# Kernel optimization log

Hardware: AMD Instinct MI355X
Metric: run time of the kernel (lower is better)

## Reference

```python
import jax, jax.numpy as jnp
import numpy as np

K0 = 16
TAU = -2.053748910631823
EPS = 1e-06


def setup_inputs() -> dict:
    key = jax.random.key(0)
    k1, k2, k3 = jax.random.split(key, 3)
    B, DIN, DOUT = 32768, 1024, 1024
    x = jax.random.normal(k1, (B, DIN), dtype=jnp.float32)
    weight = jax.random.normal(k2, (DOUT, DIN), dtype=jnp.float32) * 0.02
    bias = jax.random.normal(k3, (DOUT,), dtype=jnp.float32) * 0.02
    return {"x": x, "weight": weight, "bias": bias}


def reference(x, weight, bias):
    # Kernel loads x and w as fp16 and accumulates in fp32.
    x16 = x.astype(jnp.float16)        # [B, DIN]
    w16 = weight.astype(jnp.float16)   # [DOUT, DIN]

    xa, wa = x16[:, :K0], w16[:, :K0]
    # Warmup partial dot product over the first K0 columns: y1[b,n] = sum_k x[b,k]*w[n,k]
    y1 = jnp.einsum("bk,nk->bn", xa, wa, preferred_element_type=jnp.float32)
    # s2[b,n] = sum_k (x[b,k]*w[n,k])^2 = sum_k x^2 * w^2
    s2 = jnp.einsum("bk,nk->bn", xa * xa, wa * wa, preferred_element_type=jnp.float32)

    denom = jnp.sqrt(s2 / (K0 + EPS) + EPS)
    tstat = jnp.abs(y1) / jnp.maximum(denom, EPS)
    passed = tstat < TAU                     # early-terminate mask (true => skip remaining cols)
    still_active = ~passed                   # [B, DOUT]

    # Remaining columns contribute only where still_active.
    rest = jnp.einsum("bk,nk->bn", x16[:, K0:], w16[:, K0:], preferred_element_type=jnp.float32)
    acc = y1 + rest * still_active.astype(jnp.float32)

    out = acc + bias.astype(jnp.float32)
    return out.astype(x.dtype)
```

## Files before the change

kernel.cpp:

```cpp
#include <hip/hip_runtime.h>

typedef _Float16 f16;
typedef f16 f16x2 __attribute__((ext_vector_type(2)));
typedef f16 f16x4 __attribute__((ext_vector_type(4)));
typedef f16 f16x8 __attribute__((ext_vector_type(8)));
typedef float f32x4 __attribute__((ext_vector_type(4)));

constexpr int Mdim = 32768, Ndim = 1024, Kdim = 1024;
constexpr int BM = 256, BN = 256, BK = 64;
constexpr int NT = Kdim / BK;

static __device__ inline f16x2 cvt2(float a, float b) {
    return __builtin_bit_cast(f16x2, __builtin_amdgcn_cvt_pkrtz(a, b));
}
static __device__ inline f16x4 cvt4(float4 v) {
    f16x2 lo = cvt2(v.x, v.y), hi = cvt2(v.z, v.w);
    return __builtin_shufflevector(lo, hi, 0, 1, 2, 3);
}

__global__ __launch_bounds__(512, 2)
void etrow_gemm(const float* __restrict__ X, const float* __restrict__ W,
                const float* __restrict__ bias, float* __restrict__ out)
{
    __shared__ f16 As[2][BM * BK];
    __shared__ f16 Bs[2][BN * BK];

    const int bid = blockIdx.x;
    const int cpx = gridDim.x >> 3;
    const int wg  = (bid & 7) * cpx + (bid >> 3);
    const int mIdx = wg >> 2;
    const int nIdx = wg & 3;

    const int tid  = threadIdx.x;
    const int lane = tid & 63;
    const int wave = tid >> 6;
    const int wr   = (wave >> 2) * 128;
    const int wc   = (wave & 3) * 64;

    const int r0 = tid >> 4;
    const int c4 = tid & 15;

    const float* Xb = X + (size_t)mIdx * BM * Kdim;
    const float* Wb = W + (size_t)nIdx * BN * Kdim;

    float4 S[8];
    f32x4 acc[8][4] = {};

    auto loadA = [&](int kt) {
        const float* xa = Xb + kt * BK + c4 * 4;
        #pragma unroll
        for (int p = 0; p < 8; ++p)
            S[p] = *(const float4*)(xa + (p * 32 + r0) * Kdim);
    };
    auto loadB = [&](int kt) {
        const float* wb = Wb + kt * BK + c4 * 4;
        #pragma unroll
        for (int p = 0; p < 8; ++p)
            S[p] = *(const float4*)(wb + (p * 32 + r0) * Kdim);
    };
    auto cvtWrite = [&](f16* lds) {
        #pragma unroll
        for (int p = 0; p < 8; ++p) {
            const int r = p * 32 + r0;
            const int byte = (r * (BK * 2) + c4 * 8) ^ ((r & 7) << 4);
            *(f16x4*)((char*)lds + byte) = cvt4(S[p]);
        }
    };

    auto computeSub = [&](const f16* Ab, const f16* Bb, int s) {
        f16x8 af[8], bf[4];
        const int kb = s * 64 + (lane >> 4) * 16;
        #pragma unroll
        for (int i = 0; i < 8; ++i) {
            const int r = wr + i * 16 + (lane & 15);
            const int byte = (r * (BK * 2) + kb) ^ ((r & 7) << 4);
            af[i] = *(const f16x8*)((const char*)Ab + byte);
        }
        #pragma unroll
        for (int j = 0; j < 4; ++j) {
            const int r = wc + j * 16 + (lane & 15);
            const int byte = (r * (BK * 2) + kb) ^ ((r & 7) << 4);
            bf[j] = *(const f16x8*)((const char*)Bb + byte);
        }
        #pragma unroll
        for (int i = 0; i < 8; ++i)
            #pragma unroll
            for (int j = 0; j < 4; ++j)
                acc[i][j] = __builtin_amdgcn_mfma_f32_16x16x32_f16(
                    af[i], bf[j], acc[i][j], 0, 0, 0);
    };

    loadA(0); cvtWrite(&As[0][0]);
    loadB(0); cvtWrite(&Bs[0][0]);
    loadA(1);
    __syncthreads();

    for (int t = 0; t < NT; ++t) {
        const int cur = t & 1, nxt = cur ^ 1;
        if (t + 1 < NT) { cvtWrite(&As[nxt][0]); loadB(t + 1); }
        computeSub(&As[cur][0], &Bs[cur][0], 0);
        if (t + 1 < NT) { cvtWrite(&Bs[nxt][0]); }
        if (t + 2 < NT) { loadA(t + 2); }
        computeSub(&As[cur][0], &Bs[cur][0], 1);
        __syncthreads();
    }

    const int col0  = nIdx * BN + wc + (lane & 15);
    const int rbase = mIdx * BM + wr + (lane >> 4) * 4;
    float bv[4];
    #pragma unroll
    for (int n = 0; n < 4; ++n) bv[n] = bias[col0 + n * 16];

    #pragma unroll
    for (int m = 0; m < 8; ++m) {
        #pragma unroll
        for (int j = 0; j < 4; ++j) {
            const int row = rbase + m * 16 + j;
            float* o = out + (size_t)row * Ndim + col0;
            #pragma unroll
            for (int n = 0; n < 4; ++n)
                o[n * 16] = acc[m][n][j] + bv[n];
        }
    }
}

extern "C" void kernel_launch(void* const* d_in, const int* in_sizes, int n_in,
                              void* d_out, int out_size, void* d_ws, size_t ws_size,
                              hipStream_t stream) {
    const float* X  = (const float*)d_in[0];
    const float* W  = (const float*)d_in[1];
    const float* bs = (const float*)d_in[2];
    float* out = (float*)d_out;
    const int grid = (Mdim / BM) * (Ndim / BN);
    etrow_gemm<<<grid, 512, 0, stream>>>(X, W, bs, out);
}
```

Measured before the change: 96.74 us.

## Restructure K-loop into four barrier-synchronized phases with MFMA priority boosting

Splits each K-tile's compute into four phases of two 16-row sub-tiles, with workgroup barriers and s_setprio raised around the MFMA bursts. The A and B global loads, conversions and LDS writes for the next tile are interleaved between those phases. A and B staging now use separate register arrays (SA/SB), so both next-tile loads can be in flight at once. The aim is to hide global-load and LDS-write latency behind matrix work and keep waves in lockstep. In exchange it adds more barriers per tile and more registers, which risks spills or lower occupancy.

After: 150.6 us. +55.6%, slower.

```diff
diff --git a/kernel.cpp b/kernel.cpp
--- a/kernel.cpp
+++ b/kernel.cpp
@@ -16,6 +16,11 @@
 static __device__ inline f16x4 cvt4(float4 v) {
     f16x2 lo = cvt2(v.x, v.y), hi = cvt2(v.z, v.w);
     return __builtin_shufflevector(lo, hi, 0, 1, 2, 3);
+}
+static __device__ inline void bar() {
+    asm volatile("" ::: "memory");
+    __builtin_amdgcn_s_barrier();
+    asm volatile("" ::: "memory");
 }
 
 __global__ __launch_bounds__(512, 2)
@@ -43,66 +48,90 @@
     const float* Xb = X + (size_t)mIdx * BM * Kdim;
     const float* Wb = W + (size_t)nIdx * BN * Kdim;
 
-    float4 S[8];
+    float4 SA[8], SB[8];
     f32x4 acc[8][4] = {};
 
-    auto loadA = [&](int kt) {
-        const float* xa = Xb + kt * BK + c4 * 4;
+    auto issueA = [&](int kt) {
+        const float* p = Xb + kt * BK + c4 * 4;
         #pragma unroll
-        for (int p = 0; p < 8; ++p)
-            S[p] = *(const float4*)(xa + (p * 32 + r0) * Kdim);
+        for (int q = 0; q < 8; ++q)
+            SA[q] = *(const float4*)(p + (q * 32 + r0) * Kdim);
     };
-    auto loadB = [&](int kt) {
-        const float* wb = Wb + kt * BK + c4 * 4;
+    auto issueB = [&](int kt) {
+        const float* p = Wb + kt * BK + c4 * 4;
         #pragma unroll
-        for (int p = 0; p < 8; ++p)
-            S[p] = *(const float4*)(wb + (p * 32 + r0) * Kdim);
+        for (int q = 0; q < 8; ++q)
+            SB[q] = *(const float4*)(p + (q * 32 + r0) * Kdim);
     };
-    auto cvtWrite = [&](f16* lds) {
+    auto cvtWrA = [&](f16* lds) {
         #pragma unroll
-        for (int p = 0; p < 8; ++p) {
-            const int r = p * 32 + r0;
-            const int byte = (r * (BK * 2) + c4 * 8) ^ ((r & 7) << 4);
-            *(f16x4*)((char*)lds + byte) = cvt4(S[p]);
+        for (int q = 0; q < 8; ++q) {
+            const int r = q * 32 + r0;
+            const int byte = (r * 128 + c4 * 8) ^ ((r & 7) << 4);
+            *(f16x4*)((char*)lds + byte) = cvt4(SA[q]);
+        }
+    };
+    auto cvtWrB = [&](f16* lds) {
+        #pragma unroll
+        for (int q = 0; q < 8; ++q) {
+            const int r = q * 32 + r0;
+            const int byte = (r * 128 + c4 * 8) ^ ((r & 7) << 4);
+            *(f16x4*)((char*)lds + byte) = cvt4(SB[q]);
         }
     };
 
-    auto computeSub = [&](const f16* Ab, const f16* Bb, int s) {
-        f16x8 af[8], bf[4];
-        const int kb = s * 64 + (lane >> 4) * 16;
+    auto phase = [&](const f16* Ac, const f16* Bc, int m0) {
+        f16x8 af[2][2];
         #pragma unroll
-        for (int i = 0; i < 8; ++i) {
-            const int r = wr + i * 16 + (lane & 15);
-            const int byte = (r * (BK * 2) + kb) ^ ((r & 7) << 4);
-            af[i] = *(const f16x8*)((const char*)Ab + byte);
+        for (int mi = 0; mi < 2; ++mi)
+            #pragma unroll
+            for (int s = 0; s < 2; ++s) {
+                const int r = wr + (m0 + mi) * 16 + (lane & 15);
+                const int byte = (r * 128 + s * 64 + (lane >> 4) * 16) ^ ((r & 7) << 4);
+                af[mi][s] = *(const f16x8*)((const char*)Ac + byte);
+            }
+        bar();
+        __builtin_amdgcn_s_setprio(1);
+        #pragma unroll
+        for (int s = 0; s < 2; ++s) {
+            f16x8 bf[4];
+            #pragma unroll
+            for (int j = 0; j < 4; ++j) {
+                const int r = wc + j * 16 + (lane & 15);
+                const int byte = (r * 128 + s * 64 + (lane >> 4) * 16) ^ ((r & 7) << 4);
+                bf[j] = *(const f16x8*)((const char*)Bc + byte);
+            }
+            #pragma unroll
+            for (int mi = 0; mi < 2; ++mi)
+                #pragma unroll
+                for (int j = 0; j < 4; ++j)
+                    acc[m0 + mi][j] = __builtin_amdgcn_mfma_f32_16x16x32_f16(
+                        af[mi][s], bf[j], acc[m0 + mi][j], 0, 0, 0);
         }
-        #pragma unroll
-        for (int j = 0; j < 4; ++j) {
-            const int r = wc + j * 16 + (lane & 15);
-            const int byte = (r * (BK * 2) + kb) ^ ((r & 7) << 4);
-            bf[j] = *(const f16x8*)((const char*)Bb + byte);
-        }
-        #pragma unroll
-        for (int i = 0; i < 8; ++i)
-            #pragma unroll
-            for (int j = 0; j < 4; ++j)
-                acc[i][j] = __builtin_amdgcn_mfma_f32_16x16x32_f16(
-                    af[i], bf[j], acc[i][j], 0, 0, 0);
+        __builtin_amdgcn_s_setprio(0);
+        bar();
     };
 
-    loadA(0); cvtWrite(&As[0][0]);
-    loadB(0); cvtWrite(&Bs[0][0]);
-    loadA(1);
-    __syncthreads();
+    issueA(0); cvtWrA(&As[0][0]);
+    issueB(0); cvtWrB(&Bs[0][0]);
+    asm volatile("s_waitcnt lgkmcnt(0)" ::: "memory");
+    bar();
 
     for (int t = 0; t < NT; ++t) {
-        const int cur = t & 1, nxt = cur ^ 1;
-        if (t + 1 < NT) { cvtWrite(&As[nxt][0]); loadB(t + 1); }
-        computeSub(&As[cur][0], &Bs[cur][0], 0);
-        if (t + 1 < NT) { cvtWrite(&Bs[nxt][0]); }
-        if (t + 2 < NT) { loadA(t + 2); }
-        computeSub(&As[cur][0], &Bs[cur][0], 1);
-        __syncthreads();
+        const int cur = t & 1;
+        f16* Ac = &As[cur][0];     f16* Bc = &Bs[cur][0];
+        f16* An = &As[cur ^ 1][0]; f16* Bn = &Bs[cur ^ 1][0];
+        const bool hn = (t + 1) < NT;
+
+        if (hn) issueA(t + 1);
+        phase(Ac, Bc, 0);
+        if (hn) issueB(t + 1);
+        phase(Ac, Bc, 2);
+        if (hn) cvtWrA(An);
+        phase(Ac, Bc, 4);
+        if (hn) cvtWrB(Bn);
+        asm volatile("s_waitcnt lgkmcnt(0)" ::: "memory");
+        phase(Ac, Bc, 6);
     }
 
     const int col0  = nIdx * BN + wc + (lane & 15);
```
